# Kernel tuning notes

Measured on AMD Instinct MI355X. Metric: run time of the kernel, lower is better.

Reference implementation:

```python
import jax, jax.numpy as jnp
import numpy as np

B = 8          # number of subgraphs (seq_start_end rows)
N = 2048       # nodes per subgraph (equal-size segments)
D = 64         # h_dim
H = 4          # gat_heads
ALPHA = 0.2    # leaky relu slope


def setup_inputs() -> dict:
    key = jax.random.key(0)
    k1, k2, k3, k4, k5 = jax.random.split(key, 5)
    h_states = jax.random.normal(k1, (B * N, D), dtype=jnp.float32)
    # xavier-ish scales
    W_heads = jax.random.normal(k2, (H, D, D), dtype=jnp.float32) * (1.414 * np.sqrt(2.0 / (D + D)))
    a_heads = jax.random.normal(k3, (H, 2 * D), dtype=jnp.float32) * (1.414 * np.sqrt(2.0 / (2 * D + 1)))
    W_out = jax.random.normal(k4, (H * D, D), dtype=jnp.float32) * (1.414 * np.sqrt(2.0 / (H * D + D)))
    a_out = jax.random.normal(k5, (2 * D,), dtype=jnp.float32) * (1.414 * np.sqrt(2.0 / (2 * D + 1)))
    starts = jnp.arange(B, dtype=jnp.int32) * N
    seq_start_end = jnp.stack([starts, starts + N], axis=1)  # (B, 2)
    return {"h_states": h_states, "W_heads": W_heads, "a_heads": a_heads,
            "W_out": W_out, "a_out": a_out, "seq_start_end": seq_start_end}


def _gat_layer(x, W, a):
    """Dense GAT layer. Equivalent to the torch.cat O(N^2*2d) construction,
    rewritten as separate a1/a2 projections + broadcast add. Eval mode (no dropout)."""
    h = x @ W                      # (N, dout)
    d = W.shape[1]
    s1 = h @ a[:d]                 # (N,)  score contribution of source node i
    s2 = h @ a[d:]                 # (N,)  score contribution of target node j
    e = jax.nn.leaky_relu(s1[:, None] + s2[None, :], ALPHA)  # (N, N)
    attn = jax.nn.softmax(e, axis=1)
    return attn @ h                # (N, dout)


def reference(h_states, W_heads, a_heads, W_out, a_out, seq_start_end):
    # seq_start_end encodes B equal contiguous segments of length N -> reshape
    x = h_states.reshape(B, N, D)

    def per_graph(xg):  # xg: (N, D)
        # multi-head attention layers, concat=True -> elu on each head output
        hp = jax.vmap(lambda W, a: jax.nn.elu(_gat_layer(xg, W, a)))(W_heads, a_heads)  # (H, N, D)
        xc = jnp.transpose(hp, (1, 0, 2)).reshape(N, H * D)
        # output attention layer, concat=False (no elu inside), then elu + log_softmax outside
        out = jax.nn.elu(_gat_layer(xc, W_out, a_out))   # (N, D)
        return jax.nn.log_softmax(out, axis=1)

    return jax.vmap(per_graph)(x).reshape(B * N, D)
```

## Files before the change

kernel.cpp:

```cpp
#include <hip/hip_runtime.h>
#include <math.h>

#define NTOT 16384
#define NSEG 2048

#define OFF_HH   0ull
#define OFF_XC   4194304ull
#define OFF_S1H  8388608ull
#define OFF_S2H  8454144ull
#define OFF_S1O  8519680ull
#define OFF_S2O  8536064ull
#define OFF_SVAL 8552448ull
#define OFF_WN   8617984ull
#define OFF_SIDX 8683520ull
#define OFF_VAS  8749056ull
#define OFF_CSA  9277440ull
#define OFF_CSS  9281568ull
#define OFF_SCA  9285696ull
#define OFF_SCS  9351232ull
#define OFF_AS   9416768ull

__device__ inline unsigned long long pack_key(float v, int idx) {
    unsigned u = __float_as_uint(v);
    u = (u & 0x80000000u) ? ~u : (u | 0x80000000u);
    return ((unsigned long long)u << 32) | (unsigned)idx;
}
__device__ inline float unpack_key(unsigned long long k) {
    unsigned u = (unsigned)(k >> 32);
    u = (u & 0x80000000u) ? (u ^ 0x80000000u) : ~u;
    return __uint_as_float(u);
}
__device__ inline unsigned long long shfl_xor_u64(unsigned long long x, int mask) {
    unsigned lo = (unsigned)x, hi = (unsigned)(x >> 32);
    lo = (unsigned)__shfl_xor((int)lo, mask, 64);
    hi = (unsigned)__shfl_xor((int)hi, mask, 64);
    return ((unsigned long long)hi << 32) | lo;
}

__global__ __launch_bounds__(256) void gemm1_k(const float* __restrict__ X,
                                               const float* __restrict__ Wh,
                                               const float* __restrict__ aH,
                                               float* __restrict__ hh,
                                               float* __restrict__ s1h,
                                               float* __restrict__ s2h) {
    __shared__ float As[64][68];
    __shared__ float Bs[64][68];
    const int tid = threadIdx.x;
    const int bm = blockIdx.x, h = blockIdx.y;
    const int c0 = tid & 63, r0 = tid >> 6;
#pragma unroll
    for (int r = 0; r < 16; ++r) {
        int row = r0 + r * 4;
        As[c0][row] = X[(size_t)(bm * 64 + row) * 64 + c0];
        Bs[row][c0] = Wh[h * 4096 + row * 64 + c0];
    }
    __syncthreads();
    const int tx = tid & 15, ty = tid >> 4;
    const int m0 = ty * 4, n0 = tx * 4;
    float acc[4][4] = {};
#pragma unroll
    for (int kk = 0; kk < 64; ++kk) {
        float4 a = *(const float4*)&As[kk][m0];
        float4 b = *(const float4*)&Bs[kk][n0];
        acc[0][0] += a.x * b.x; acc[0][1] += a.x * b.y; acc[0][2] += a.x * b.z; acc[0][3] += a.x * b.w;
        acc[1][0] += a.y * b.x; acc[1][1] += a.y * b.y; acc[1][2] += a.y * b.z; acc[1][3] += a.y * b.w;
        acc[2][0] += a.z * b.x; acc[2][1] += a.z * b.y; acc[2][2] += a.z * b.z; acc[2][3] += a.z * b.w;
        acc[3][0] += a.w * b.x; acc[3][1] += a.w * b.y; acc[3][2] += a.w * b.z; acc[3][3] += a.w * b.w;
    }
    const int g = bm >> 5;
    const int nb = (bm * 64) & 2047;
#pragma unroll
    for (int i = 0; i < 4; ++i) {
        float4 v = make_float4(acc[i][0], acc[i][1], acc[i][2], acc[i][3]);
        *(float4*)&hh[(((size_t)h * 8 + g) * NSEG + nb + m0 + i) * 64 + n0] = v;
    }
#pragma unroll
    for (int i = 0; i < 4; ++i) {
        float p1 = 0.f, p2 = 0.f;
#pragma unroll
        for (int jj = 0; jj < 4; ++jj) {
            p1 += acc[i][jj] * aH[h * 128 + n0 + jj];
            p2 += acc[i][jj] * aH[h * 128 + 64 + n0 + jj];
        }
#pragma unroll
        for (int off = 8; off; off >>= 1) {
            p1 += __shfl_xor(p1, off, 16);
            p2 += __shfl_xor(p2, off, 16);
        }
        if (tx == 0) {
            s1h[h * NTOT + bm * 64 + m0 + i] = p1;
            s2h[h * NTOT + bm * 64 + m0 + i] = p2;
        }
    }
}

__global__ __launch_bounds__(256) void gemm2_k(const float* __restrict__ XC,
                                               const float* __restrict__ Wo,
                                               const float* __restrict__ aO,
                                               float* __restrict__ hc,
                                               float* __restrict__ s1o,
                                               float* __restrict__ s2o) {
    __shared__ float As[64][34];
    __shared__ float Bs[64][68];
    const int tid = threadIdx.x;
    const int bm = blockIdx.x;
    const int c0 = tid & 63, r0 = tid >> 6;
    const int tx = tid & 15, ty = tid >> 4;
    const int m0 = ty * 2, n0 = tx * 4;
    float acc[2][4] = {};
    for (int kt = 0; kt < 4; ++kt) {
#pragma unroll
        for (int r = 0; r < 8; ++r) {
            int row = r0 + r * 4;
            As[c0][row] = XC[(size_t)(bm * 32 + row) * 256 + kt * 64 + c0];
        }
#pragma unroll
        for (int r = 0; r < 16; ++r) {
            int row = r0 + r * 4;
            Bs[row][c0] = Wo[(kt * 64 + row) * 64 + c0];
        }
        __syncthreads();
#pragma unroll
        for (int kk = 0; kk < 64; ++kk) {
            float2 a = *(const float2*)&As[kk][m0];
            float4 b = *(const float4*)&Bs[kk][n0];
            acc[0][0] += a.x * b.x; acc[0][1] += a.x * b.y; acc[0][2] += a.x * b.z; acc[0][3] += a.x * b.w;
            acc[1][0] += a.y * b.x; acc[1][1] += a.y * b.y; acc[1][2] += a.y * b.z; acc[1][3] += a.y * b.w;
        }
        __syncthreads();
    }
#pragma unroll
    for (int i = 0; i < 2; ++i) {
        float4 v = make_float4(acc[i][0], acc[i][1], acc[i][2], acc[i][3]);
        *(float4*)&hc[(size_t)(bm * 32 + m0 + i) * 64 + n0] = v;
    }
#pragma unroll
    for (int i = 0; i < 2; ++i) {
        float p1 = 0.f, p2 = 0.f;
#pragma unroll
        for (int jj = 0; jj < 4; ++jj) {
            p1 += acc[i][jj] * aO[n0 + jj];
            p2 += acc[i][jj] * aO[64 + n0 + jj];
        }
#pragma unroll
        for (int off = 8; off; off >>= 1) {
            p1 += __shfl_xor(p1, off, 16);
            p2 += __shfl_xor(p2, off, 16);
        }
        if (tx == 0) {
            s1o[bm * 32 + m0 + i] = p1;
            s2o[bm * 32 + m0 + i] = p2;
        }
    }
}

__global__ __launch_bounds__(1024) void sort_k(const float* __restrict__ s2_all,
                                               int heads,
                                               float* __restrict__ g_sval,
                                               int* __restrict__ g_sidx,
                                               float* __restrict__ g_wN) {
    __shared__ unsigned long long sA[2][1024];
    __shared__ unsigned long long sB[2][1024];
    __shared__ float sM2;
    const int tid = threadIdx.x, t = blockIdx.x;
    const int g = t / heads, h = t % heads;
    const float* s2p = s2_all + (size_t)h * NTOT + (size_t)g * NSEG;

    unsigned long long a0 = pack_key(s2p[tid], tid);
    unsigned long long a1 = pack_key(s2p[tid + 1024], tid + 1024);
    int p = 0;
    for (int k = 2; k <= 2048; k <<= 1) {
        const bool up0 = (tid & k) == 0;
        const bool up1 = (((tid + 1024) & k) == 0);
        for (int j = k >> 1; j > 0; j >>= 1) {
            if (j >= 1024) {
                unsigned long long lo = a0 < a1 ? a0 : a1;
                unsigned long long hi = a0 < a1 ? a1 : a0;
                a0 = up0 ? lo : hi;
                a1 = up0 ? hi : lo;
            } else if (j >= 64) {
                sA[p][tid] = a0; sB[p][tid] = a1;
                __syncthreads();
                unsigned long long q0 = sA[p][tid ^ j], q1 = sB[p][tid ^ j];
                bool lower = (tid & j) == 0;
                a0 = ((a0 < q0) == (lower == up0)) ? a0 : q0;
                a1 = ((a1 < q1) == (lower == up1)) ? a1 : q1;
                p ^= 1;
            } else {
                unsigned long long q0 = shfl_xor_u64(a0, j);
                unsigned long long q1 = shfl_xor_u64(a1, j);
                bool lower = (tid & j) == 0;
                a0 = ((a0 < q0) == (lower == up0)) ? a0 : q0;
                a1 = ((a1 < q1) == (lower == up1)) ? a1 : q1;
            }
        }
    }
    float v0 = unpack_key(a0), v1 = unpack_key(a1);
    if (tid == 1023) sM2 = v1;
    __syncthreads();
    const float M2 = sM2;
    int i0 = (int)(unsigned)(a0 & 0xffffffffu);
    int i1 = (int)(unsigned)(a1 & 0xffffffffu);
    float w0 = __expf(0.2f * (v0 - M2));
    float w1 = __expf(0.2f * (v1 - M2));
    size_t o = (size_t)t * NSEG;
    g_sval[o + tid] = v0; g_sval[o + tid + 1024] = v1;
    g_sidx[o + tid] = i0; g_sidx[o + tid + 1024] = i1;
    g_wN[o + tid] = w0;   g_wN[o + tid + 1024] = w1;
}

__global__ __launch_bounds__(256) void tabw_k(const float* __restrict__ V,
                                              int heads, int ntask,
                                              const int* __restrict__ g_sidx,
                                              const float* __restrict__ g_wN,
                                              float* __restrict__ AS,
                                              float* __restrict__ SCA, float* __restrict__ SCS,
                                              float* __restrict__ TAS,
                                              float* __restrict__ TSA, float* __restrict__ TSS) {
    const int L = blockIdx.x + (int)(gridDim.x * blockIdx.y);
    const int xcd = L & 7, slot = L >> 3;
    const int tpx = ntask >> 3;
    const int t = xcd * tpx + (slot >> 5);
    const int u = slot & 31;
    const int wv = threadIdx.x >> 6, lane = threadIdx.x & 63;
    const int c = u * 4 + wv, base = c * 16;
    const int g = t / heads, h = t % heads;
    const int seg = h * (ntask / heads) + g;
    const float* Vp = V + (size_t)seg * NSEG * 64;
    const int* sidx = g_sidx + (size_t)t * NSEG + base;
    const float* wnp = g_wN + (size_t)t * NSEG + base;
    float wn[16], vv[16];
#pragma unroll
    for (int j = 0; j < 16; ++j) wn[j] = wnp[j];
#pragma unroll
    for (int j = 0; j < 16; ++j) vv[j] = Vp[(size_t)sidx[j] * 64 + lane];
    float* ASp = AS + (size_t)t * NSEG * 128;
    float accA = 0.f, scaA = 0.f;
#pragma unroll
    for (int j = 0; j < 16; ++j) {
        size_t pos = base + j;
        ASp[pos * 128 + lane] = accA;
        if (lane == 0) SCA[(size_t)t * NSEG + pos] = scaA;
        accA += wn[j] * vv[j]; scaA += wn[j];
    }
    TAS[((size_t)t * 128 + c) * 128 + lane] = accA;
    if (lane == 0) TSA[t * 128 + c] = scaA;
    float accS = 0.f, scaS = 0.f;
#pragma unroll
    for (int j = 15; j >= 0; --j) {
        float w = wn[j], w2 = w * w, wp = w2 * w2 * w;
        accS += wp * vv[j]; scaS += wp;
        size_t pos = base + j;
        ASp[pos * 128 + 64 + lane] = accS;
        if (lane == 0) SCS[(size_t)t * NSEG + pos] = scaS;
    }
    TAS[((size_t)t * 128 + c) * 128 + 64 + lane] = accS;
    if (lane == 0) TSS[t * 128 + c] = scaS;
}

__global__ __launch_bounds__(256) void scan_k(const float* __restrict__ TAS,
                                              const float* __restrict__ TSA,
                                              const float* __restrict__ TSS,
                                              float* __restrict__ VAS,
                                              float* __restrict__ CSA, float* __restrict__ CSS) {
    const int t = blockIdx.x, tid = threadIdx.x;
    const float* T = TAS + (size_t)t * 128 * 128;
    float* Vo = VAS + (size_t)t * 129 * 128;
    if (tid < 64) {
        float run = 0.f;
#pragma unroll 4
        for (int c = 0; c < 128; ++c) { Vo[c * 128 + tid] = run; run += T[c * 128 + tid]; }
        Vo[128 * 128 + tid] = run;
    } else if (tid < 128) {
        float run = 0.f;
#pragma unroll 4
        for (int c = 127; c >= 0; --c) { Vo[c * 128 + tid] = run; run += T[c * 128 + tid]; }
    } else if (tid == 128) {
        float run = 0.f;
        for (int c = 0; c < 128; ++c) { CSA[t * 129 + c] = run; run += TSA[t * 128 + c]; }
        CSA[t * 129 + 128] = run;
    } else if (tid == 129) {
        float run = 0.f;
        for (int c = 127; c >= 0; --c) { CSS[t * 129 + c] = run; run += TSS[t * 128 + c]; }
    }
}

template <int MODE>
__global__ __launch_bounds__(256) void query_k(const float* __restrict__ s1_all,
                                               float* __restrict__ out,
                                               int heads, int ntask, int ostride,
                                               const float* __restrict__ g_sval,
                                               const float* __restrict__ AS,
                                               const float* __restrict__ SCA, const float* __restrict__ SCS,
                                               const float* __restrict__ VAS,
                                               const float* __restrict__ CSA, const float* __restrict__ CSS) {
    __shared__ float sval[NSEG];
    const int tid = threadIdx.x;
    const int L = blockIdx.x + (int)(gridDim.x * blockIdx.y);
    const int xcd = L & 7, slot = L >> 3;
    const int tpx = ntask >> 3;
    const int t = xcd * tpx + (slot >> 5);
    const int u = slot & 31;
    const int g = t / heads, h = t % heads;
    const float4* sv4 = (const float4*)(g_sval + (size_t)t * NSEG);
    for (int i = tid; i < NSEG / 4; i += 256) ((float4*)sval)[i] = sv4[i];
    __syncthreads();
    const float M2 = sval[NSEG - 1];
    const int lane = tid & 63, wv = tid >> 6;
    const int q0 = u * 64 + wv * 16;
    const float* s1p = s1_all + (size_t)h * NTOT + (size_t)g * NSEG;
    float* outp = out + (size_t)g * NSEG * ostride + h * 64;
    const float* ASp = AS + (size_t)t * NSEG * 128;
    const float* VASp = VAS + (size_t)t * 129 * 128;
    const float* scA = SCA + (size_t)t * NSEG;
    const float* scS = SCS + (size_t)t * NSEG;
    const float* csA = CSA + (size_t)t * 129;
    const float* csS = CSS + (size_t)t * 129;
    int myq = q0 + (lane & 15);
    float s1v = s1p[myq];
    float th = -s1v;
    int lo = 0, hi = NSEG;
    while (lo < hi) { int mid = (lo + hi) >> 1; if (sval[mid] <= th) lo = mid + 1; else hi = mid; }
#pragma unroll 4
    for (int j = 0; j < 16; ++j) {
        int k = __shfl(lo, j, 64);
        float s1q = __shfl(s1v, j, 64);
        float accA, scaA, accS, scaS;
        if (k < NSEG) {
            const int c = k >> 4;
            const float* rowP = ASp + (size_t)k * 128;
            const float* rowC = VASp + (size_t)c * 128;
            accA = rowP[lane] + rowC[lane];
            accS = rowP[64 + lane] + rowC[64 + lane];
            scaA = scA[k] + csA[c];
            scaS = scS[k] + csS[c];
        } else {
            accA = VASp[128 * 128 + lane]; scaA = csA[128];
            accS = 0.f; scaS = 0.f;
        }
        float cc = __expf(-0.8f * fmaxf(s1q + M2, 0.f));
        float o = (accS + cc * accA) / (scaS + cc * scaA);
        o = o > 0.f ? o : expm1f(o);
        int q = q0 + j;
        if (MODE == 0) {
            outp[(size_t)q * ostride + lane] = o;
        } else {
            float m = o;
#pragma unroll
            for (int off = 32; off; off >>= 1) m = fmaxf(m, __shfl_xor(m, off, 64));
            float e = __expf(o - m);
#pragma unroll
            for (int off = 32; off; off >>= 1) e += __shfl_xor(e, off, 64);
            outp[(size_t)q * ostride + lane] = o - m - __logf(e);
        }
    }
}

extern "C" void kernel_launch(void* const* d_in, const int* in_sizes, int n_in,
                              void* d_out, int out_size, void* d_ws, size_t ws_size,
                              hipStream_t stream) {
    const float* h_states = (const float*)d_in[0];
    const float* W_heads = (const float*)d_in[1];
    const float* a_heads = (const float*)d_in[2];
    const float* W_out = (const float*)d_in[3];
    const float* a_out = (const float*)d_in[4];
    float* w = (float*)d_ws;
    float* hh = w + OFF_HH;
    float* xc = w + OFF_XC;
    float* hc = w + OFF_HH;
    float* s1h = w + OFF_S1H;
    float* s2h = w + OFF_S2H;
    float* s1o = w + OFF_S1O;
    float* s2o = w + OFF_S2O;
    float* g_sval = w + OFF_SVAL;
    float* g_wN = w + OFF_WN;
    int* g_sidx = (int*)(w + OFF_SIDX);
    float* TAS = w + OFF_XC;
    float* TSA = w + OFF_XC + 524288;
    float* TSS = w + OFF_XC + 528384;
    float* VAS = w + OFF_VAS;
    float* CSA = w + OFF_CSA;
    float* CSS = w + OFF_CSS;
    float* SCA = w + OFF_SCA;
    float* SCS = w + OFF_SCS;
    float* AS = w + OFF_AS;
    float* outp = (float*)d_out;

    gemm1_k<<<dim3(256, 4), 256, 0, stream>>>(h_states, W_heads, a_heads, hh, s1h, s2h);
    sort_k<<<32, 1024, 0, stream>>>(s2h, 4, g_sval, g_sidx, g_wN);
    tabw_k<<<dim3(32, 32), 256, 0, stream>>>(hh, 4, 32, g_sidx, g_wN, AS, SCA, SCS, TAS, TSA, TSS);
    scan_k<<<32, 256, 0, stream>>>(TAS, TSA, TSS, VAS, CSA, CSS);
    query_k<0><<<dim3(32, 32), 256, 0, stream>>>(s1h, xc, 4, 32, 256, g_sval, AS, SCA, SCS, VAS, CSA, CSS);
    gemm2_k<<<512, 256, 0, stream>>>(xc, W_out, a_out, hc, s1o, s2o);
    sort_k<<<8, 1024, 0, stream>>>(s2o, 1, g_sval, g_sidx, g_wN);
    tabw_k<<<dim3(32, 8), 256, 0, stream>>>(hc, 1, 8, g_sidx, g_wN, AS, SCA, SCS, TAS, TSA, TSS);
    scan_k<<<8, 256, 0, stream>>>(TAS, TSA, TSS, VAS, CSA, CSS);
    query_k<1><<<dim3(32, 8), 256, 0, stream>>>(s1o, outp, 1, 8, 64, g_sval, AS, SCA, SCS, VAS, CSA, CSS);
}
```

Before: 199.4 us.

## Fuse all ten stage kernels into one cooperative persistent kernel with grid syncs

Replaces the ten separate kernel launches (gemm, sort, table build, scan, query for both GAT layers) with a single cooperative kernel of 256 blocks of 1024 threads, separated by grid.sync barriers. Each stage's body is turned into a device function and work is remapped onto the fixed grid, with several 256-thread tiles packed per block. This removes launch gaps and inter-kernel drain overhead. In exchange, stages with little parallelism (sorts, scans on 8–32 blocks) leave most blocks idle at barriers, occupancy is limited by the large shared allocation and 1024-thread blocks, and grid syncs carry their own cost.

```diff
diff --git a/kernel.cpp b/kernel.cpp
--- a/kernel.cpp
+++ b/kernel.cpp
@@ -1,5 +1,8 @@
 #include <hip/hip_runtime.h>
+#include <hip/hip_cooperative_groups.h>
 #include <math.h>
+
+namespace cg = cooperative_groups;
 
 #define NTOT 16384
 #define NSEG 2048
@@ -37,196 +40,13 @@
     return ((unsigned long long)hi << 32) | lo;
 }
 
-__global__ __launch_bounds__(256) void gemm1_k(const float* __restrict__ X,
-                                               const float* __restrict__ Wh,
-                                               const float* __restrict__ aH,
-                                               float* __restrict__ hh,
-                                               float* __restrict__ s1h,
-                                               float* __restrict__ s2h) {
-    __shared__ float As[64][68];
-    __shared__ float Bs[64][68];
-    const int tid = threadIdx.x;
-    const int bm = blockIdx.x, h = blockIdx.y;
-    const int c0 = tid & 63, r0 = tid >> 6;
-#pragma unroll
-    for (int r = 0; r < 16; ++r) {
-        int row = r0 + r * 4;
-        As[c0][row] = X[(size_t)(bm * 64 + row) * 64 + c0];
-        Bs[row][c0] = Wh[h * 4096 + row * 64 + c0];
-    }
-    __syncthreads();
-    const int tx = tid & 15, ty = tid >> 4;
-    const int m0 = ty * 4, n0 = tx * 4;
-    float acc[4][4] = {};
-#pragma unroll
-    for (int kk = 0; kk < 64; ++kk) {
-        float4 a = *(const float4*)&As[kk][m0];
-        float4 b = *(const float4*)&Bs[kk][n0];
-        acc[0][0] += a.x * b.x; acc[0][1] += a.x * b.y; acc[0][2] += a.x * b.z; acc[0][3] += a.x * b.w;
-        acc[1][0] += a.y * b.x; acc[1][1] += a.y * b.y; acc[1][2] += a.y * b.z; acc[1][3] += a.y * b.w;
-        acc[2][0] += a.z * b.x; acc[2][1] += a.z * b.y; acc[2][2] += a.z * b.z; acc[2][3] += a.z * b.w;
-        acc[3][0] += a.w * b.x; acc[3][1] += a.w * b.y; acc[3][2] += a.w * b.z; acc[3][3] += a.w * b.w;
-    }
-    const int g = bm >> 5;
-    const int nb = (bm * 64) & 2047;
-#pragma unroll
-    for (int i = 0; i < 4; ++i) {
-        float4 v = make_float4(acc[i][0], acc[i][1], acc[i][2], acc[i][3]);
-        *(float4*)&hh[(((size_t)h * 8 + g) * NSEG + nb + m0 + i) * 64 + n0] = v;
-    }
-#pragma unroll
-    for (int i = 0; i < 4; ++i) {
-        float p1 = 0.f, p2 = 0.f;
-#pragma unroll
-        for (int jj = 0; jj < 4; ++jj) {
-            p1 += acc[i][jj] * aH[h * 128 + n0 + jj];
-            p2 += acc[i][jj] * aH[h * 128 + 64 + n0 + jj];
-        }
-#pragma unroll
-        for (int off = 8; off; off >>= 1) {
-            p1 += __shfl_xor(p1, off, 16);
-            p2 += __shfl_xor(p2, off, 16);
-        }
-        if (tx == 0) {
-            s1h[h * NTOT + bm * 64 + m0 + i] = p1;
-            s2h[h * NTOT + bm * 64 + m0 + i] = p2;
-        }
-    }
-}
-
-__global__ __launch_bounds__(256) void gemm2_k(const float* __restrict__ XC,
-                                               const float* __restrict__ Wo,
-                                               const float* __restrict__ aO,
-                                               float* __restrict__ hc,
-                                               float* __restrict__ s1o,
-                                               float* __restrict__ s2o) {
-    __shared__ float As[64][34];
-    __shared__ float Bs[64][68];
-    const int tid = threadIdx.x;
-    const int bm = blockIdx.x;
-    const int c0 = tid & 63, r0 = tid >> 6;
-    const int tx = tid & 15, ty = tid >> 4;
-    const int m0 = ty * 2, n0 = tx * 4;
-    float acc[2][4] = {};
-    for (int kt = 0; kt < 4; ++kt) {
-#pragma unroll
-        for (int r = 0; r < 8; ++r) {
-            int row = r0 + r * 4;
-            As[c0][row] = XC[(size_t)(bm * 32 + row) * 256 + kt * 64 + c0];
-        }
-#pragma unroll
-        for (int r = 0; r < 16; ++r) {
-            int row = r0 + r * 4;
-            Bs[row][c0] = Wo[(kt * 64 + row) * 64 + c0];
-        }
-        __syncthreads();
-#pragma unroll
-        for (int kk = 0; kk < 64; ++kk) {
-            float2 a = *(const float2*)&As[kk][m0];
-            float4 b = *(const float4*)&Bs[kk][n0];
-            acc[0][0] += a.x * b.x; acc[0][1] += a.x * b.y; acc[0][2] += a.x * b.z; acc[0][3] += a.x * b.w;
-            acc[1][0] += a.y * b.x; acc[1][1] += a.y * b.y; acc[1][2] += a.y * b.z; acc[1][3] += a.y * b.w;
-        }
-        __syncthreads();
-    }
-#pragma unroll
-    for (int i = 0; i < 2; ++i) {
-        float4 v = make_float4(acc[i][0], acc[i][1], acc[i][2], acc[i][3]);
-        *(float4*)&hc[(size_t)(bm * 32 + m0 + i) * 64 + n0] = v;
-    }
-#pragma unroll
-    for (int i = 0; i < 2; ++i) {
-        float p1 = 0.f, p2 = 0.f;
-#pragma unroll
-        for (int jj = 0; jj < 4; ++jj) {
-            p1 += acc[i][jj] * aO[n0 + jj];
-            p2 += acc[i][jj] * aO[64 + n0 + jj];
-        }
-#pragma unroll
-        for (int off = 8; off; off >>= 1) {
-            p1 += __shfl_xor(p1, off, 16);
-            p2 += __shfl_xor(p2, off, 16);
-        }
-        if (tx == 0) {
-            s1o[bm * 32 + m0 + i] = p1;
-            s2o[bm * 32 + m0 + i] = p2;
-        }
-    }
-}
-
-__global__ __launch_bounds__(1024) void sort_k(const float* __restrict__ s2_all,
-                                               int heads,
-                                               float* __restrict__ g_sval,
-                                               int* __restrict__ g_sidx,
-                                               float* __restrict__ g_wN) {
-    __shared__ unsigned long long sA[2][1024];
-    __shared__ unsigned long long sB[2][1024];
-    __shared__ float sM2;
-    const int tid = threadIdx.x, t = blockIdx.x;
-    const int g = t / heads, h = t % heads;
-    const float* s2p = s2_all + (size_t)h * NTOT + (size_t)g * NSEG;
-
-    unsigned long long a0 = pack_key(s2p[tid], tid);
-    unsigned long long a1 = pack_key(s2p[tid + 1024], tid + 1024);
-    int p = 0;
-    for (int k = 2; k <= 2048; k <<= 1) {
-        const bool up0 = (tid & k) == 0;
-        const bool up1 = (((tid + 1024) & k) == 0);
-        for (int j = k >> 1; j > 0; j >>= 1) {
-            if (j >= 1024) {
-                unsigned long long lo = a0 < a1 ? a0 : a1;
-                unsigned long long hi = a0 < a1 ? a1 : a0;
-                a0 = up0 ? lo : hi;
-                a1 = up0 ? hi : lo;
-            } else if (j >= 64) {
-                sA[p][tid] = a0; sB[p][tid] = a1;
-                __syncthreads();
-                unsigned long long q0 = sA[p][tid ^ j], q1 = sB[p][tid ^ j];
-                bool lower = (tid & j) == 0;
-                a0 = ((a0 < q0) == (lower == up0)) ? a0 : q0;
-                a1 = ((a1 < q1) == (lower == up1)) ? a1 : q1;
-                p ^= 1;
-            } else {
-                unsigned long long q0 = shfl_xor_u64(a0, j);
-                unsigned long long q1 = shfl_xor_u64(a1, j);
-                bool lower = (tid & j) == 0;
-                a0 = ((a0 < q0) == (lower == up0)) ? a0 : q0;
-                a1 = ((a1 < q1) == (lower == up1)) ? a1 : q1;
-            }
-        }
-    }
-    float v0 = unpack_key(a0), v1 = unpack_key(a1);
-    if (tid == 1023) sM2 = v1;
-    __syncthreads();
-    const float M2 = sM2;
-    int i0 = (int)(unsigned)(a0 & 0xffffffffu);
-    int i1 = (int)(unsigned)(a1 & 0xffffffffu);
-    float w0 = __expf(0.2f * (v0 - M2));
-    float w1 = __expf(0.2f * (v1 - M2));
-    size_t o = (size_t)t * NSEG;
-    g_sval[o + tid] = v0; g_sval[o + tid + 1024] = v1;
-    g_sidx[o + tid] = i0; g_sidx[o + tid + 1024] = i1;
-    g_wN[o + tid] = w0;   g_wN[o + tid + 1024] = w1;
-}
-
-__global__ __launch_bounds__(256) void tabw_k(const float* __restrict__ V,
-                                              int heads, int ntask,
-                                              const int* __restrict__ g_sidx,
-                                              const float* __restrict__ g_wN,
-                                              float* __restrict__ AS,
-                                              float* __restrict__ SCA, float* __restrict__ SCS,
-                                              float* __restrict__ TAS,
-                                              float* __restrict__ TSA, float* __restrict__ TSS) {
-    const int L = blockIdx.x + (int)(gridDim.x * blockIdx.y);
-    const int xcd = L & 7, slot = L >> 3;
-    const int tpx = ntask >> 3;
-    const int t = xcd * tpx + (slot >> 5);
-    const int u = slot & 31;
-    const int wv = threadIdx.x >> 6, lane = threadIdx.x & 63;
-    const int c = u * 4 + wv, base = c * 16;
-    const int g = t / heads, h = t % heads;
-    const int seg = h * (ntask / heads) + g;
-    const float* Vp = V + (size_t)seg * NSEG * 64;
+__device__ __forceinline__ void tabw_body(const float* __restrict__ Vp, int t, int c, int lane,
+                                          const int* __restrict__ g_sidx, const float* __restrict__ g_wN,
+                                          float* __restrict__ AS,
+                                          float* __restrict__ SCA, float* __restrict__ SCS,
+                                          float* __restrict__ TAS,
+                                          float* __restrict__ TSA, float* __restrict__ TSS) {
+    const int base = c * 16;
     const int* sidx = g_sidx + (size_t)t * NSEG + base;
     const float* wnp = g_wN + (size_t)t * NSEG + base;
     float wn[16], vv[16];
@@ -248,7 +68,7 @@
     float accS = 0.f, scaS = 0.f;
 #pragma unroll
     for (int j = 15; j >= 0; --j) {
-        float w = wn[j], w2 = w * w, wp = w2 * w2 * w;
+        float wq = wn[j], w2 = wq * wq, wp = w2 * w2 * wq;
         accS += wp * vv[j]; scaS += wp;
         size_t pos = base + j;
         ASp[pos * 128 + 64 + lane] = accS;
@@ -258,12 +78,11 @@
     if (lane == 0) TSS[t * 128 + c] = scaS;
 }
 
-__global__ __launch_bounds__(256) void scan_k(const float* __restrict__ TAS,
-                                              const float* __restrict__ TSA,
-                                              const float* __restrict__ TSS,
-                                              float* __restrict__ VAS,
-                                              float* __restrict__ CSA, float* __restrict__ CSS) {
-    const int t = blockIdx.x, tid = threadIdx.x;
+__device__ __forceinline__ void scan_body(int t, int tid,
+                                          const float* __restrict__ TAS,
+                                          const float* __restrict__ TSA, const float* __restrict__ TSS,
+                                          float* __restrict__ VAS,
+                                          float* __restrict__ CSA, float* __restrict__ CSS) {
     const float* T = TAS + (size_t)t * 128 * 128;
     float* Vo = VAS + (size_t)t * 129 * 128;
     if (tid < 64) {
@@ -286,30 +105,14 @@
 }
 
 template <int MODE>
-__global__ __launch_bounds__(256) void query_k(const float* __restrict__ s1_all,
-                                               float* __restrict__ out,
-                                               int heads, int ntask, int ostride,
-                                               const float* __restrict__ g_sval,
-                                               const float* __restrict__ AS,
-                                               const float* __restrict__ SCA, const float* __restrict__ SCS,
-                                               const float* __restrict__ VAS,
-                                               const float* __restrict__ CSA, const float* __restrict__ CSS) {
-    __shared__ float sval[NSEG];
-    const int tid = threadIdx.x;
-    const int L = blockIdx.x + (int)(gridDim.x * blockIdx.y);
-    const int xcd = L & 7, slot = L >> 3;
-    const int tpx = ntask >> 3;
-    const int t = xcd * tpx + (slot >> 5);
-    const int u = slot & 31;
-    const int g = t / heads, h = t % heads;
-    const float4* sv4 = (const float4*)(g_sval + (size_t)t * NSEG);
-    for (int i = tid; i < NSEG / 4; i += 256) ((float4*)sval)[i] = sv4[i];
-    __syncthreads();
-    const float M2 = sval[NSEG - 1];
-    const int lane = tid & 63, wv = tid >> 6;
-    const int q0 = u * 64 + wv * 16;
-    const float* s1p = s1_all + (size_t)h * NTOT + (size_t)g * NSEG;
-    float* outp = out + (size_t)g * NSEG * ostride + h * 64;
+__device__ __forceinline__ void query_body(int t, int q0, int lane, float M2,
+                                           const float* __restrict__ sval,
+                                           const float* __restrict__ s1p,
+                                           float* __restrict__ outp, int ostride,
+                                           const float* __restrict__ AS,
+                                           const float* __restrict__ SCA, const float* __restrict__ SCS,
+                                           const float* __restrict__ VAS,
+                                           const float* __restrict__ CSA, const float* __restrict__ CSS) {
     const float* ASp = AS + (size_t)t * NSEG * 128;
     const float* VASp = VAS + (size_t)t * 129 * 128;
     const float* scA = SCA + (size_t)t * NSEG;
@@ -356,15 +159,66 @@
     }
 }
 
-extern "C" void kernel_launch(void* const* d_in, const int* in_sizes, int n_in,
-                              void* d_out, int out_size, void* d_ws, size_t ws_size,
-                              hipStream_t stream) {
-    const float* h_states = (const float*)d_in[0];
-    const float* W_heads = (const float*)d_in[1];
-    const float* a_heads = (const float*)d_in[2];
-    const float* W_out = (const float*)d_in[3];
-    const float* a_out = (const float*)d_in[4];
-    float* w = (float*)d_ws;
+__device__ __forceinline__ void sort_body(const float* __restrict__ s2p, int t, int tid,
+                                          unsigned long long* sA, unsigned long long* sB, float* sM2,
+                                          float* __restrict__ g_sval, int* __restrict__ g_sidx,
+                                          float* __restrict__ g_wN) {
+    unsigned long long a0 = pack_key(s2p[tid], tid);
+    unsigned long long a1 = pack_key(s2p[tid + 1024], tid + 1024);
+    int p = 0;
+    for (int k = 2; k <= 2048; k <<= 1) {
+        const bool up0 = (tid & k) == 0;
+        const bool up1 = (((tid + 1024) & k) == 0);
+        for (int j = k >> 1; j > 0; j >>= 1) {
+            if (j >= 1024) {
+                unsigned long long lo = a0 < a1 ? a0 : a1;
+                unsigned long long hi = a0 < a1 ? a1 : a0;
+                a0 = up0 ? lo : hi;
+                a1 = up0 ? hi : lo;
+            } else if (j >= 64) {
+                sA[p * 1024 + tid] = a0; sB[p * 1024 + tid] = a1;
+                __syncthreads();
+                unsigned long long q0 = sA[p * 1024 + (tid ^ j)], q1 = sB[p * 1024 + (tid ^ j)];
+                bool lower = (tid & j) == 0;
+                a0 = ((a0 < q0) == (lower == up0)) ? a0 : q0;
+                a1 = ((a1 < q1) == (lower == up1)) ? a1 : q1;
+                p ^= 1;
+            } else {
+                unsigned long long q0 = shfl_xor_u64(a0, j);
+                unsigned long long q1 = shfl_xor_u64(a1, j);
+                bool lower = (tid & j) == 0;
+                a0 = ((a0 < q0) == (lower == up0)) ? a0 : q0;
+                a1 = ((a1 < q1) == (lower == up1)) ? a1 : q1;
+            }
+        }
+    }
+    float v0 = unpack_key(a0), v1 = unpack_key(a1);
+    if (tid == 1023) *sM2 = v1;
+    __syncthreads();
+    const float M2 = *sM2;
+    int i0 = (int)(unsigned)(a0 & 0xffffffffu);
+    int i1 = (int)(unsigned)(a1 & 0xffffffffu);
+    float w0 = __expf(0.2f * (v0 - M2));
+    float w1 = __expf(0.2f * (v1 - M2));
+    size_t o = (size_t)t * NSEG;
+    g_sval[o + tid] = v0; g_sval[o + tid + 1024] = v1;
+    g_sidx[o + tid] = i0; g_sidx[o + tid + 1024] = i1;
+    g_wN[o + tid] = w0;   g_wN[o + tid + 1024] = w1;
+}
+
+__global__ __launch_bounds__(1024) void mega_k(const float* __restrict__ X,
+                                               const float* __restrict__ Wh,
+                                               const float* __restrict__ aH,
+                                               const float* __restrict__ Wo,
+                                               const float* __restrict__ aO,
+                                               float* __restrict__ w,
+                                               float* __restrict__ outg) {
+    cg::grid_group grid = cg::this_grid();
+    __shared__ __align__(16) char smem[139264];
+    __shared__ float sM2;
+    const int tid = threadIdx.x;
+    const int blk = blockIdx.x;
+
     float* hh = w + OFF_HH;
     float* xc = w + OFF_XC;
     float* hc = w + OFF_HH;
@@ -384,16 +238,218 @@
     float* SCA = w + OFF_SCA;
     float* SCS = w + OFF_SCS;
     float* AS = w + OFF_AS;
+
+    {
+        const int sub = tid >> 8, st = tid & 255;
+        const int tile = sub * 256 + blk;
+        const int h = tile & 3, bm = tile >> 2;
+        float (*As)[68] = (float (*)[68])(smem + (size_t)sub * 34816);
+        float (*Bs)[68] = (float (*)[68])(smem + (size_t)sub * 34816 + 17408);
+        const int c0 = st & 63, r0 = st >> 6;
+#pragma unroll
+        for (int r = 0; r < 16; ++r) {
+            int row = r0 + r * 4;
+            As[c0][row] = X[(size_t)(bm * 64 + row) * 64 + c0];
+            Bs[row][c0] = Wh[h * 4096 + row * 64 + c0];
+        }
+        __syncthreads();
+        const int tx = st & 15, ty = st >> 4;
+        const int m0 = ty * 4, n0 = tx * 4;
+        float acc[4][4] = {};
+#pragma unroll
+        for (int kk = 0; kk < 64; ++kk) {
+            float4 a = *(const float4*)&As[kk][m0];
+            float4 b = *(const float4*)&Bs[kk][n0];
+            acc[0][0] += a.x * b.x; acc[0][1] += a.x * b.y; acc[0][2] += a.x * b.z; acc[0][3] += a.x * b.w;
+            acc[1][0] += a.y * b.x; acc[1][1] += a.y * b.y; acc[1][2] += a.y * b.z; acc[1][3] += a.y * b.w;
+            acc[2][0] += a.z * b.x; acc[2][1] += a.z * b.y; acc[2][2] += a.z * b.z; acc[2][3] += a.z * b.w;
+            acc[3][0] += a.w * b.x; acc[3][1] += a.w * b.y; acc[3][2] += a.w * b.z; acc[3][3] += a.w * b.w;
+        }
+        const int g = bm >> 5;
+        const int nb = (bm * 64) & 2047;
+#pragma unroll
+        for (int i = 0; i < 4; ++i) {
+            float4 v = make_float4(acc[i][0], acc[i][1], acc[i][2], acc[i][3]);
+            *(float4*)&hh[(((size_t)h * 8 + g) * NSEG + nb + m0 + i) * 64 + n0] = v;
+        }
+#pragma unroll
+        for (int i = 0; i < 4; ++i) {
+            float p1 = 0.f, p2 = 0.f;
+#pragma unroll
+            for (int jj = 0; jj < 4; ++jj) {
+                p1 += acc[i][jj] * aH[h * 128 + n0 + jj];
+                p2 += acc[i][jj] * aH[h * 128 + 64 + n0 + jj];
+            }
+#pragma unroll
+            for (int off = 8; off; off >>= 1) {
+                p1 += __shfl_xor(p1, off, 16);
+                p2 += __shfl_xor(p2, off, 16);
+            }
+            if (tx == 0) {
+                s1h[h * NTOT + bm * 64 + m0 + i] = p1;
+                s2h[h * NTOT + bm * 64 + m0 + i] = p2;
+            }
+        }
+    }
+    grid.sync();
+
+    if (blk < 32) {
+        unsigned long long* sA = (unsigned long long*)smem;
+        unsigned long long* sB = sA + 2048;
+        const int t = blk, g = t >> 2, h = t & 3;
+        sort_body(s2h + (size_t)h * NTOT + (size_t)g * NSEG, t, tid, sA, sB, &sM2,
+                  g_sval, g_sidx, g_wN);
+    }
+    grid.sync();
+
+    {
+        const int wv = tid >> 6, lane = tid & 63;
+        const int chunk = blk * 16 + wv;
+        const int t = chunk >> 7, c = chunk & 127;
+        const int g = t >> 2, h = t & 3;
+        const float* Vp = hh + ((size_t)h * 8 + g) * NSEG * 64;
+        tabw_body(Vp, t, c, lane, g_sidx, g_wN, AS, SCA, SCS, TAS, TSA, TSS);
+    }
+    grid.sync();
+
+    if (blk < 32) scan_body(blk, tid, TAS, TSA, TSS, VAS, CSA, CSS);
+    grid.sync();
+
+    {
+        float* sval = (float*)smem;
+        const int t = blk >> 3, u8 = blk & 7;
+        const int g = t >> 2, h = t & 3;
+        const float4* sv4 = (const float4*)(g_sval + (size_t)t * NSEG);
+        for (int i = tid; i < NSEG / 4; i += 1024) ((float4*)sval)[i] = sv4[i];
+        __syncthreads();
+        const float M2 = sval[NSEG - 1];
+        const int lane = tid & 63, wv = tid >> 6;
+        const int q0 = u8 * 256 + wv * 16;
+        query_body<0>(t, q0, lane, M2, sval,
+                      s1h + (size_t)h * NTOT + (size_t)g * NSEG,
+                      xc + (size_t)g * NSEG * 256 + h * 64, 256,
+                      AS, SCA, SCS, VAS, CSA, CSS);
+    }
+    grid.sync();
+
+    {
+        const int sub = tid >> 8, st = tid & 255;
+        const int tile = sub * 256 + blk;
+        const bool valid = tile < 512;
+        const int bm = tile;
+        float (*As2)[34] = (float (*)[34])(smem + (size_t)sub * 26112);
+        float (*Bs2)[68] = (float (*)[68])(smem + (size_t)sub * 26112 + 8704);
+        const int c0 = st & 63, r0 = st >> 6;
+        const int tx = st & 15, ty = st >> 4;
+        const int m0 = ty * 2, n0 = tx * 4;
+        float acc[2][4] = {};
+        for (int kt = 0; kt < 4; ++kt) {
+            if (valid) {
+#pragma unroll
+                for (int r = 0; r < 8; ++r) {
+                    int row = r0 + r * 4;
+                    As2[c0][row] = xc[(size_t)(bm * 32 + row) * 256 + kt * 64 + c0];
+                }
+#pragma unroll
+                for (int r = 0; r < 16; ++r) {
+                    int row = r0 + r * 4;
+                    Bs2[row][c0] = Wo[(kt * 64 + row) * 64 + c0];
+                }
+            }
+            __syncthreads();
+            if (valid) {
+#pragma unroll
+                for (int kk = 0; kk < 64; ++kk) {
+                    float2 a = *(const float2*)&As2[kk][m0];
+                    float4 b = *(const float4*)&Bs2[kk][n0];
+                    acc[0][0] += a.x * b.x; acc[0][1] += a.x * b.y; acc[0][2] += a.x * b.z; acc[0][3] += a.x * b.w;
+                    acc[1][0] += a.y * b.x; acc[1][1] += a.y * b.y; acc[1][2] += a.y * b.z; acc[1][3] += a.y * b.w;
+                }
+            }
+            __syncthreads();
+        }
+        if (valid) {
+#pragma unroll
+            for (int i = 0; i < 2; ++i) {
+                float4 v = make_float4(acc[i][0], acc[i][1], acc[i][2], acc[i][3]);
+                *(float4*)&hc[(size_t)(bm * 32 + m0 + i) * 64 + n0] = v;
+            }
+#pragma unroll
+            for (int i = 0; i < 2; ++i) {
+                float p1 = 0.f, p2 = 0.f;
+#pragma unroll
+                for (int jj = 0; jj < 4; ++jj) {
+                    p1 += acc[i][jj] * aO[n0 + jj];
+                    p2 += acc[i][jj] * aO[64 + n0 + jj];
+                }
+#pragma unroll
+                for (int off = 8; off; off >>= 1) {
+                    p1 += __shfl_xor(p1, off, 16);
+                    p2 += __shfl_xor(p2, off, 16);
+                }
+                if (tx == 0) {
+                    s1o[bm * 32 + m0 + i] = p1;
+                    s2o[bm * 32 + m0 + i] = p2;
+                }
+            }
+        }
+    }
+    grid.sync();
+
+    if (blk < 8) {
+        unsigned long long* sA = (unsigned long long*)smem;
+        unsigned long long* sB = sA + 2048;
+        const int t = blk;
+        sort_body(s2o + (size_t)t * NSEG, t, tid, sA, sB, &sM2,
+                  g_sval, g_sidx, g_wN);
+    }
+    grid.sync();
+
+    {
+        const int wv = tid >> 6, lane = tid & 63;
+        if (wv < 4) {
+            const int chunk = blk * 4 + wv;
+            const int t = chunk >> 7, c = chunk & 127;
+            const float* Vp = hc + (size_t)t * NSEG * 64;
+            tabw_body(Vp, t, c, lane, g_sidx, g_wN, AS, SCA, SCS, TAS, TSA, TSS);
+        }
+    }
+    grid.sync();
+
+    if (blk < 8) scan_body(blk, tid, TAS, TSA, TSS, VAS, CSA, CSS);
+    grid.sync();
+
+    {
+        float* sval = (float*)smem;
+        const int t = blk >> 5, u = blk & 31;
+        const float4* sv4 = (const float4*)(g_sval + (size_t)t * NSEG);
+        for (int i = tid; i < NSEG / 4; i += 1024) ((float4*)sval)[i] = sv4[i];
+        __syncthreads();
+        const float M2 = sval[NSEG - 1];
+        const int lane = tid & 63, wv = tid >> 6;
+        if (wv < 4) {
+            const int q0 = u * 64 + wv * 16;
+            query_body<1>(t, q0, lane, M2, sval,
+                          s1o + (size_t)t * NSEG,
+                          outg + (size_t)t * NSEG * 64, 64,
+                          AS, SCA, SCS, VAS, CSA, CSS);
+        }
+    }
+}
+
+extern "C" void kernel_launch(void* const* d_in, const int* in_sizes, int n_in,
+                              void* d_out, int out_size, void* d_ws, size_t ws_size,
+                              hipStream_t stream) {
+    const float* h_states = (const float*)d_in[0];
+    const float* W_heads = (const float*)d_in[1];
+    const float* a_heads = (const float*)d_in[2];
+    const float* W_out = (const float*)d_in[3];
+    const float* a_out = (const float*)d_in[4];
+    float* w = (float*)d_ws;
     float* outp = (float*)d_out;
 
-    gemm1_k<<<dim3(256, 4), 256, 0, stream>>>(h_states, W_heads, a_heads, hh, s1h, s2h);
-    sort_k<<<32, 1024, 0, stream>>>(s2h, 4, g_sval, g_sidx, g_wN);
-    tabw_k<<<dim3(32, 32), 256, 0, stream>>>(hh, 4, 32, g_sidx, g_wN, AS, SCA, SCS, TAS, TSA, TSS);
-    scan_k<<<32, 256, 0, stream>>>(TAS, TSA, TSS, VAS, CSA, CSS);
-    query_k<0><<<dim3(32, 32), 256, 0, stream>>>(s1h, xc, 4, 32, 256, g_sval, AS, SCA, SCS, VAS, CSA, CSS);
-    gemm2_k<<<512, 256, 0, stream>>>(xc, W_out, a_out, hc, s1o, s2o);
-    sort_k<<<8, 1024, 0, stream>>>(s2o, 1, g_sval, g_sidx, g_wN);
-    tabw_k<<<dim3(32, 8), 256, 0, stream>>>(hc, 1, 8, g_sidx, g_wN, AS, SCA, SCS, TAS, TSA, TSS);
-    scan_k<<<8, 256, 0, stream>>>(TAS, TSA, TSS, VAS, CSA, CSS);
-    query_k<1><<<dim3(32, 8), 256, 0, stream>>>(s1o, outp, 1, 8, 64, g_sval, AS, SCA, SCS, VAS, CSA, CSS);
-}
+    void* args[] = {(void*)&h_states, (void*)&W_heads, (void*)&a_heads,
+                    (void*)&W_out, (void*)&a_out, (void*)&w, (void*)&outp};
+    hipLaunchCooperativeKernel((const void*)mega_k, dim3(256), dim3(1024),
+                               args, 0, stream);
+}
```

Result: slower. 446.4 us (+123.9%).

## Fuse tabulate, scan and query kernels using last-block scan with flag wait

Applied to the files above, without the earlier changes.

Merges the tabw, scan and query stages into a single kernel per GAT layer. Each task's last-arriving block, found with an atomic counter, runs the scan and then sets a release flag, while the other blocks of that task spin until the flag is set before running their queries. Counters are zeroed inside the preceding GEMM kernels, and the TAS scratch moves to its own workspace region. This removes two kernel launches and their inter-kernel gaps per layer. The cost is spin-waiting blocks, whose correctness depends on all blocks of a task being co-resident.

```diff
diff --git a/kernel.cpp b/kernel.cpp
--- a/kernel.cpp
+++ b/kernel.cpp
@@ -19,6 +19,10 @@
 #define OFF_SCA  9285696ull
 #define OFF_SCS  9351232ull
 #define OFF_AS   9416768ull
+#define OFF_CNT  17805376ull
+#define OFF_TAS  17805888ull
+#define OFF_TSA  18330176ull
+#define OFF_TSS  18334272ull
 
 __device__ inline unsigned long long pack_key(float v, int idx) {
     unsigned u = __float_as_uint(v);
@@ -42,11 +46,13 @@
                                                const float* __restrict__ aH,
                                                float* __restrict__ hh,
                                                float* __restrict__ s1h,
-                                               float* __restrict__ s2h) {
+                                               float* __restrict__ s2h,
+                                               int* __restrict__ cntbase) {
     __shared__ float As[64][68];
     __shared__ float Bs[64][68];
     const int tid = threadIdx.x;
     const int bm = blockIdx.x, h = blockIdx.y;
+    if (bm == 0 && h == 0 && tid < 160) cntbase[tid] = 0;
     const int c0 = tid & 63, r0 = tid >> 6;
 #pragma unroll
     for (int r = 0; r < 16; ++r) {
@@ -99,11 +105,13 @@
                                                const float* __restrict__ aO,
                                                float* __restrict__ hc,
                                                float* __restrict__ s1o,
-                                               float* __restrict__ s2o) {
+                                               float* __restrict__ s2o,
+                                               int* __restrict__ cnt2base) {
     __shared__ float As[64][34];
     __shared__ float Bs[64][68];
     const int tid = threadIdx.x;
     const int bm = blockIdx.x;
+    if (bm == 0 && tid < 136) cnt2base[tid] = 0;
     const int c0 = tid & 63, r0 = tid >> 6;
     const int tx = tid & 15, ty = tid >> 4;
     const int m0 = ty * 2, n0 = tx * 4;
@@ -209,24 +217,13 @@
     g_wN[o + tid] = w0;   g_wN[o + tid + 1024] = w1;
 }
 
-__global__ __launch_bounds__(256) void tabw_k(const float* __restrict__ V,
-                                              int heads, int ntask,
-                                              const int* __restrict__ g_sidx,
-                                              const float* __restrict__ g_wN,
-                                              float* __restrict__ AS,
-                                              float* __restrict__ SCA, float* __restrict__ SCS,
-                                              float* __restrict__ TAS,
-                                              float* __restrict__ TSA, float* __restrict__ TSS) {
-    const int L = blockIdx.x + (int)(gridDim.x * blockIdx.y);
-    const int xcd = L & 7, slot = L >> 3;
-    const int tpx = ntask >> 3;
-    const int t = xcd * tpx + (slot >> 5);
-    const int u = slot & 31;
-    const int wv = threadIdx.x >> 6, lane = threadIdx.x & 63;
-    const int c = u * 4 + wv, base = c * 16;
-    const int g = t / heads, h = t % heads;
-    const int seg = h * (ntask / heads) + g;
-    const float* Vp = V + (size_t)seg * NSEG * 64;
+__device__ __forceinline__ void tabw_body(const float* __restrict__ Vp, int t, int c, int lane,
+                                          const int* __restrict__ g_sidx, const float* __restrict__ g_wN,
+                                          float* __restrict__ AS,
+                                          float* __restrict__ SCA, float* __restrict__ SCS,
+                                          float* __restrict__ TAS,
+                                          float* __restrict__ TSA, float* __restrict__ TSS) {
+    const int base = c * 16;
     const int* sidx = g_sidx + (size_t)t * NSEG + base;
     const float* wnp = g_wN + (size_t)t * NSEG + base;
     float wn[16], vv[16];
@@ -248,7 +245,7 @@
     float accS = 0.f, scaS = 0.f;
 #pragma unroll
     for (int j = 15; j >= 0; --j) {
-        float w = wn[j], w2 = w * w, wp = w2 * w2 * w;
+        float wq = wn[j], w2 = wq * wq, wp = w2 * w2 * wq;
         accS += wp * vv[j]; scaS += wp;
         size_t pos = base + j;
         ASp[pos * 128 + 64 + lane] = accS;
@@ -258,12 +255,11 @@
     if (lane == 0) TSS[t * 128 + c] = scaS;
 }
 
-__global__ __launch_bounds__(256) void scan_k(const float* __restrict__ TAS,
-                                              const float* __restrict__ TSA,
-                                              const float* __restrict__ TSS,
-                                              float* __restrict__ VAS,
-                                              float* __restrict__ CSA, float* __restrict__ CSS) {
-    const int t = blockIdx.x, tid = threadIdx.x;
+__device__ __forceinline__ void scan_body(int t, int tid,
+                                          const float* __restrict__ TAS,
+                                          const float* __restrict__ TSA, const float* __restrict__ TSS,
+                                          float* __restrict__ VAS,
+                                          float* __restrict__ CSA, float* __restrict__ CSS) {
     const float* T = TAS + (size_t)t * 128 * 128;
     float* Vo = VAS + (size_t)t * 129 * 128;
     if (tid < 64) {
@@ -286,30 +282,14 @@
 }
 
 template <int MODE>
-__global__ __launch_bounds__(256) void query_k(const float* __restrict__ s1_all,
-                                               float* __restrict__ out,
-                                               int heads, int ntask, int ostride,
-                                               const float* __restrict__ g_sval,
-                                               const float* __restrict__ AS,
-                                               const float* __restrict__ SCA, const float* __restrict__ SCS,
-                                               const float* __restrict__ VAS,
-                                               const float* __restrict__ CSA, const float* __restrict__ CSS) {
-    __shared__ float sval[NSEG];
-    const int tid = threadIdx.x;
-    const int L = blockIdx.x + (int)(gridDim.x * blockIdx.y);
-    const int xcd = L & 7, slot = L >> 3;
-    const int tpx = ntask >> 3;
-    const int t = xcd * tpx + (slot >> 5);
-    const int u = slot & 31;
-    const int g = t / heads, h = t % heads;
-    const float4* sv4 = (const float4*)(g_sval + (size_t)t * NSEG);
-    for (int i = tid; i < NSEG / 4; i += 256) ((float4*)sval)[i] = sv4[i];
-    __syncthreads();
-    const float M2 = sval[NSEG - 1];
-    const int lane = tid & 63, wv = tid >> 6;
-    const int q0 = u * 64 + wv * 16;
-    const float* s1p = s1_all + (size_t)h * NTOT + (size_t)g * NSEG;
-    float* outp = out + (size_t)g * NSEG * ostride + h * 64;
+__device__ __forceinline__ void query_body(int t, int q0, int lane, float M2,
+                                           const float* __restrict__ sval,
+                                           const float* __restrict__ s1p,
+                                           float* __restrict__ outp, int ostride,
+                                           const float* __restrict__ AS,
+                                           const float* __restrict__ SCA, const float* __restrict__ SCS,
+                                           const float* __restrict__ VAS,
+                                           const float* __restrict__ CSA, const float* __restrict__ CSS) {
     const float* ASp = AS + (size_t)t * NSEG * 128;
     const float* VASp = VAS + (size_t)t * 129 * 128;
     const float* scA = SCA + (size_t)t * NSEG;
@@ -356,6 +336,68 @@
     }
 }
 
+template <int MODE>
+__global__ __launch_bounds__(256) void fused_k(const float* __restrict__ V,
+                                               int heads, int ntask,
+                                               const int* __restrict__ g_sidx,
+                                               const float* __restrict__ g_wN,
+                                               float* __restrict__ AS,
+                                               float* __restrict__ SCA, float* __restrict__ SCS,
+                                               float* __restrict__ TAS,
+                                               float* __restrict__ TSA, float* __restrict__ TSS,
+                                               float* __restrict__ VAS,
+                                               float* __restrict__ CSA, float* __restrict__ CSS,
+                                               const float* __restrict__ s1_all,
+                                               float* __restrict__ out, int ostride,
+                                               const float* __restrict__ g_sval,
+                                               int* __restrict__ cnt, int* __restrict__ flag) {
+    __shared__ float sval[NSEG];
+    __shared__ int s_last;
+    const int tid = threadIdx.x;
+    const int L = blockIdx.x;
+    const int xcd = L & 7, slot = L >> 3;
+    const int tpx = ntask >> 3;
+    const int t = xcd * tpx + (slot >> 5);
+    const int u = slot & 31;
+    const int wv = tid >> 6, lane = tid & 63;
+    const int g = t / heads, h = t % heads;
+    const int seg = h * (ntask / heads) + g;
+    const float* Vp = V + (size_t)seg * NSEG * 64;
+
+    tabw_body(Vp, t, u * 4 + wv, lane, g_sidx, g_wN, AS, SCA, SCS, TAS, TSA, TSS);
+
+    const float4* sv4 = (const float4*)(g_sval + (size_t)t * NSEG);
+    for (int i = tid; i < NSEG / 4; i += 256) ((float4*)sval)[i] = sv4[i];
+
+    __threadfence();
+    __syncthreads();
+    if (tid == 0) {
+        int old = atomicAdd(&cnt[t], 1);
+        s_last = (old == 31) ? 1 : 0;
+    }
+    __syncthreads();
+    if (s_last) {
+        __threadfence();
+        scan_body(t, tid, TAS, TSA, TSS, VAS, CSA, CSS);
+        __threadfence();
+        __syncthreads();
+        if (tid == 0) __hip_atomic_store(&flag[t], 1, __ATOMIC_RELEASE, __HIP_MEMORY_SCOPE_AGENT);
+    } else {
+        if (tid == 0) {
+            while (__hip_atomic_load(&flag[t], __ATOMIC_ACQUIRE, __HIP_MEMORY_SCOPE_AGENT) == 0)
+                __builtin_amdgcn_s_sleep(16);
+        }
+        __syncthreads();
+        __threadfence();
+    }
+
+    const float M2 = sval[NSEG - 1];
+    query_body<MODE>(t, u * 64 + wv * 16, lane, M2, sval,
+                     s1_all + (size_t)h * NTOT + (size_t)g * NSEG,
+                     out + (size_t)g * NSEG * ostride + h * 64, ostride,
+                     AS, SCA, SCS, VAS, CSA, CSS);
+}
+
 extern "C" void kernel_launch(void* const* d_in, const int* in_sizes, int n_in,
                               void* d_out, int out_size, void* d_ws, size_t ws_size,
                               hipStream_t stream) {
@@ -375,25 +417,28 @@
     float* g_sval = w + OFF_SVAL;
     float* g_wN = w + OFF_WN;
     int* g_sidx = (int*)(w + OFF_SIDX);
-    float* TAS = w + OFF_XC;
-    float* TSA = w + OFF_XC + 524288;
-    float* TSS = w + OFF_XC + 528384;
     float* VAS = w + OFF_VAS;
     float* CSA = w + OFF_CSA;
     float* CSS = w + OFF_CSS;
     float* SCA = w + OFF_SCA;
     float* SCS = w + OFF_SCS;
     float* AS = w + OFF_AS;
+    float* TAS = w + OFF_TAS;
+    float* TSA = w + OFF_TSA;
+    float* TSS = w + OFF_TSS;
+    int* cntb = (int*)(w + OFF_CNT);
+    int* cnt1 = cntb, *flag1 = cntb + 128;
+    int* cnt2 = cntb + 256, *flag2 = cntb + 384;
     float* outp = (float*)d_out;
 
-    gemm1_k<<<dim3(256, 4), 256, 0, stream>>>(h_states, W_heads, a_heads, hh, s1h, s2h);
+    gemm1_k<<<dim3(256, 4), 256, 0, stream>>>(h_states, W_heads, a_heads, hh, s1h, s2h, cntb);
     sort_k<<<32, 1024, 0, stream>>>(s2h, 4, g_sval, g_sidx, g_wN);
-    tabw_k<<<dim3(32, 32), 256, 0, stream>>>(hh, 4, 32, g_sidx, g_wN, AS, SCA, SCS, TAS, TSA, TSS);
-    scan_k<<<32, 256, 0, stream>>>(TAS, TSA, TSS, VAS, CSA, CSS);
-    query_k<0><<<dim3(32, 32), 256, 0, stream>>>(s1h, xc, 4, 32, 256, g_sval, AS, SCA, SCS, VAS, CSA, CSS);
-    gemm2_k<<<512, 256, 0, stream>>>(xc, W_out, a_out, hc, s1o, s2o);
+    fused_k<0><<<1024, 256, 0, stream>>>(hh, 4, 32, g_sidx, g_wN, AS, SCA, SCS,
+                                         TAS, TSA, TSS, VAS, CSA, CSS,
+                                         s1h, xc, 256, g_sval, cnt1, flag1);
+    gemm2_k<<<512, 256, 0, stream>>>(xc, W_out, a_out, hc, s1o, s2o, cntb + 256);
     sort_k<<<8, 1024, 0, stream>>>(s2o, 1, g_sval, g_sidx, g_wN);
-    tabw_k<<<dim3(32, 8), 256, 0, stream>>>(hc, 1, 8, g_sidx, g_wN, AS, SCA, SCS, TAS, TSA, TSS);
-    scan_k<<<8, 256, 0, stream>>>(TAS, TSA, TSS, VAS, CSA, CSS);
-    query_k<1><<<dim3(32, 8), 256, 0, stream>>>(s1o, outp, 1, 8, 64, g_sval, AS, SCA, SCS, VAS, CSA, CSS);
-}
+    fused_k<1><<<256, 256, 0, stream>>>(hc, 1, 8, g_sidx, g_wN, AS, SCA, SCS,
+                                        TAS, TSA, TSS, VAS, CSA, CSS,
+                                        s1o, outp, 64, g_sval, cnt2, flag2);
+}
```

Measured after the change: 614.6 us. +208.2%, slower.
